# Kernel optimization log

Hardware: AMD Instinct MI355X
Metric: run time of the kernel (lower is better)

## Reference

```python
import jax, jax.numpy as jnp
import numpy as np

# --- static config (mirrors init_kwargs) ---
B, N, CBEV = 4, 4, 64
D, FH, FW = 41, 16, 44          # depth bins, feature H/W after downsample
OGH, OGW, DS = 256, 704, 16     # original image dims, downsample
NX, NY, NZ = 240, 240, 1        # BEV grid (x, y, z)
DX = np.array([0.4, 0.4, 20.0], np.float32)            # voxel size
BX = np.array([-47.8, -47.8, 0.0], np.float32)          # voxel grid origin (bound+dx/2)


def _frustum():
    # [D, FH, FW, 3] with (u_pixel, v_pixel, depth); UD discretization 4..44 step 1
    ds = (4.0 + np.arange(D, dtype=np.float32)).reshape(D, 1, 1) * np.ones((1, FH, FW), np.float32)
    xs = np.linspace(0.0, OGW - 1, FW, dtype=np.float32).reshape(1, 1, FW) * np.ones((D, FH, 1), np.float32)
    ys = np.linspace(0.0, OGH - 1, FH, dtype=np.float32).reshape(1, FH, 1) * np.ones((D, 1, FW), np.float32)
    return jnp.asarray(np.stack([xs, ys, ds], axis=-1))


def setup_inputs() -> dict:
    key = jax.random.key(0)
    x = jax.random.normal(key, (B, N, D, FH, FW, CBEV), dtype=jnp.float32)
    # realistic camera rig: 4 cameras at yaw 0/90/180/270 deg, pinhole intrinsics
    intr = np.zeros((N, 3, 3), np.float32)
    rot = np.zeros((N, 3, 3), np.float32)
    tr = np.zeros((N, 3), np.float32)
    cam2ego = np.array([[0, 0, 1], [-1, 0, 0], [0, -1, 0]], np.float32)  # cam z-fwd -> ego x-fwd
    for n in range(N):
        intr[n] = np.array([[500.0, 0.0, OGW / 2.0], [0.0, 500.0, OGH / 2.0], [0.0, 0.0, 1.0]], np.float32)
        yaw = 2.0 * np.pi * n / N
        c, s = np.cos(yaw), np.sin(yaw)
        Rz = np.array([[c, -s, 0], [s, c, 0], [0, 0, 1]], np.float32)
        rot[n] = Rz @ cam2ego
        tr[n] = np.array([1.5 * c, 1.5 * s, 1.6], np.float32)
    rots = jnp.asarray(np.broadcast_to(rot, (B, N, 3, 3)).copy())
    trans = jnp.asarray(np.broadcast_to(tr, (B, N, 3)).copy())
    intrins = jnp.asarray(np.broadcast_to(intr, (B, N, 3, 3)).copy())
    post_rots = jnp.asarray(np.broadcast_to(np.eye(3, dtype=np.float32), (B, N, 3, 3)).copy())
    post_trans = jnp.zeros((B, N, 3), jnp.float32)
    return {"x": x, "rots": rots, "trans": trans, "intrins": intrins,
            "post_rots": post_rots, "post_trans": post_trans}


def reference(x, rots, trans, intrins, post_rots, post_trans):
    # --- get_geometry: frustum pixel/depth points -> ego-frame xyz ---
    frustum = _frustum()                                            # [D,FH,FW,3]
    pts = frustum[None, None] - post_trans[:, :, None, None, None, :]
    pts = jnp.einsum('bnij,bndhwj->bndhwi', jnp.linalg.inv(post_rots), pts)
    pts = jnp.concatenate([pts[..., :2] * pts[..., 2:3], pts[..., 2:3]], axis=-1)
    combine = rots @ jnp.linalg.inv(intrins)
    pts = jnp.einsum('bnij,bndhwj->bndhwi', combine, pts) + trans[:, :, None, None, None, :]
    # --- voxel_pooling: quantize, mask OOB, segment-sum into dense BEV grid ---
    dx = jnp.asarray(DX)
    bx = jnp.asarray(BX)
    vox = ((pts - (bx - dx / 2.0)) / dx).astype(jnp.int32)          # trunc, same as torch .long()
    vx, vy, vz = vox[..., 0], vox[..., 1], vox[..., 2]              # [B,N,D,FH,FW]
    kept = (vx >= 0) & (vx < NX) & (vy >= 0) & (vy < NY) & (vz >= 0) & (vz < NZ)
    bidx = jnp.arange(B, dtype=jnp.int32)[:, None, None, None, None]
    nvox = B * NZ * NY * NX
    lin = bidx * (NZ * NY * NX) + vz * (NY * NX) + vy * NX + vx
    lin = jnp.where(kept, lin, nvox).reshape(-1)                    # invalid -> dummy bin
    feats = x.reshape(-1, CBEV)                                     # [Nprime, C]
    sums = jax.ops.segment_sum(feats, lin, num_segments=nvox + 1)[:nvox]
    final = sums.reshape(B, NZ, NY, NX, CBEV).transpose(0, 1, 4, 2, 3)  # [B,Z,C,Y,X]
    # torch: cat(final.unbind(dim=2), 1) on [B,C,Z,Y,X] -> [B, Z*C, Y, X] z-major
    return final.reshape(B, NZ * CBEV, NY, NX)
```

## Files before the change

kernel.cpp:

```cpp
#include <hip/hip_runtime.h>

#define BB   4
#define NNC  4
#define DDEP 41
#define FHH  16
#define FWW  44
#define CC   64
#define NXX  240
#define NYY  240
#define NVOX (BB*NYY*NXX)
#define NTRI (BB*NNC*DDEP*FWW)
#define SLOTS 8

#define W_CNT  0
#define W_TAB  (NVOX)

typedef float f4 __attribute__((ext_vector_type(4)));

__device__ __forceinline__ void inv3x3_upper_f32(const float K[9], float o[9]) {
    float a00 = __fdiv_rn(1.0f, K[0]);
    float a11 = __fdiv_rn(1.0f, K[4]);
    float a22 = __fdiv_rn(1.0f, K[8]);
    float b01 = __fmul_rn(-a11, __fmul_rn(a00, K[1]));
    float x0 = __fadd_rn(__fmul_rn(a00, K[2]), __fmul_rn(b01, K[5]));
    float x1 = __fmul_rn(a11, K[5]);
    float b02 = __fmul_rn(-a22, x0);
    float b12 = __fmul_rn(-a22, x1);
    o[0]=a00; o[1]=b01; o[2]=b02;
    o[3]=0.0f; o[4]=a11; o[5]=b12;
    o[6]=0.0f; o[7]=0.0f; o[8]=a22;
}

__global__ void __launch_bounds__(256) geom(
        const float* __restrict__ rots,
        const float* __restrict__ trans,
        const float* __restrict__ intrins,
        const float* __restrict__ post_rots,
        const float* __restrict__ post_trans,
        unsigned int* __restrict__ cntp,
        unsigned int* __restrict__ table) {
    int wid  = threadIdx.x >> 6;
    int lane = threadIdx.x & 63;
    int sub  = lane >> 4;
    int h    = lane & 15;
    int tri  = (blockIdx.x*4 + wid)*4 + sub;

    int w    = tri % FWW;
    int rest = tri / FWW;
    int d    = rest % DDEP;
    int bn   = rest / DDEP;

    float K[9], PR[9], R[9];
    #pragma unroll
    for (int i = 0; i < 9; ++i) {
        K[i]  = intrins[bn*9 + i];
        PR[i] = post_rots[bn*9 + i];
        R[i]  = rots[bn*9 + i];
    }
    float Ki[9], PRi[9];
    inv3x3_upper_f32(K, Ki);
    inv3x3_upper_f32(PR, PRi);
    float C[9];
    #pragma unroll
    for (int i = 0; i < 3; ++i)
        #pragma unroll
        for (int j = 0; j < 3; ++j) {
            float s = __fmul_rn(R[i*3+0], Ki[0*3+j]);
            s = __fadd_rn(s, __fmul_rn(R[i*3+1], Ki[1*3+j]));
            s = __fadd_rn(s, __fmul_rn(R[i*3+2], Ki[2*3+j]));
            C[i*3+j] = s;
        }
    float ptx = post_trans[bn*3+0], pty = post_trans[bn*3+1], ptz = post_trans[bn*3+2];
    float trx = trans[bn*3+0], try_ = trans[bn*3+1], trz = trans[bn*3+2];

    float u  = (float)((double)w * (703.0/43.0));
    float v  = (float)((double)h * 17.0);
    float dd = (float)(4 + d);

    float p0x = __fsub_rn(u,  ptx);
    float p0y = __fsub_rn(v,  pty);
    float p0z = __fsub_rn(dd, ptz);
    float p1x = __fadd_rn(__fadd_rn(__fmul_rn(PRi[0],p0x), __fmul_rn(PRi[1],p0y)), __fmul_rn(PRi[2],p0z));
    float p1y = __fadd_rn(__fadd_rn(__fmul_rn(PRi[3],p0x), __fmul_rn(PRi[4],p0y)), __fmul_rn(PRi[5],p0z));
    float p1z = __fadd_rn(__fadd_rn(__fmul_rn(PRi[6],p0x), __fmul_rn(PRi[7],p0y)), __fmul_rn(PRi[8],p0z));
    float p2x = __fmul_rn(p1x, p1z);
    float p2y = __fmul_rn(p1y, p1z);
    float p2z = p1z;
    float ex = __fadd_rn(__fadd_rn(__fmul_rn(C[0],p2x), __fmul_rn(C[1],p2y)), __fmul_rn(C[2],p2z));
    float ey = __fadd_rn(__fadd_rn(__fmul_rn(C[3],p2x), __fmul_rn(C[4],p2y)), __fmul_rn(C[5],p2z));
    float ez = __fadd_rn(__fadd_rn(__fmul_rn(C[6],p2x), __fmul_rn(C[7],p2y)), __fmul_rn(C[8],p2z));
    float gx = __fadd_rn(ex, trx);
    float gy = __fadd_rn(ey, try_);
    float gz = __fadd_rn(ez, trz);

    float qx = __fdiv_rn(__fsub_rn(gx, -48.0f), 0.4f);
    float qy = __fdiv_rn(__fsub_rn(gy, -48.0f), 0.4f);
    float qz = __fdiv_rn(__fsub_rn(gz, -10.0f), 20.0f);
    int vx = (int)qx;
    int vy = (int)qy;
    int vz = (int)qz;

    bool kept = (vx >= 0) & (vx < NXX) & (vy >= 0) & (vy < NYY) & (vz == 0);
    unsigned long long bal = __ballot(kept);
    unsigned int mask = (unsigned int)((bal >> (sub*16)) & 0xFFFFull);

    if (h == 0 && mask != 0) {
        int b  = bn / NNC;
        int vb = b*(NYY*NXX) + vy*NXX + vx;
        unsigned int sh  = 8u*(vb & 3);
        unsigned int old = atomicAdd(&cntp[vb >> 2], 1u << sh);
        unsigned int sl  = (old >> sh) & 0xFFu;
        if (sl < SLOTS) table[vb*SLOTS + sl] = ((unsigned int)tri << 16) | mask;
    }
}

__global__ void __launch_bounds__(256) assemble(
        const float* __restrict__ x,
        const unsigned int* __restrict__ cntp,
        const unsigned int* __restrict__ table,
        float* __restrict__ out) {
    __shared__ float lds[16*68];
    int tid = threadIdx.x;
    int v0  = blockIdx.x*16;

    const uint4 cq = *(const uint4*)(cntp + (v0 >> 2));

    int b  = v0 / (NYY*NXX);
    int yx = v0 % (NYY*NXX);
    int c  = tid >> 2, q = tid & 3;
    float* outp = out + (size_t)b*(CC*NYY*NXX) + (size_t)c*(NYY*NXX) + yx + q*4;

    if ((cq.x | cq.y | cq.z | cq.w) == 0u) {
        f4 z = (f4)(0.0f);
        __builtin_nontemporal_store(z, (f4*)outp);
        return;
    }

    int wid  = tid >> 6;
    int lane = tid & 63;
    int hq   = lane >> 4;
    int c4   = lane & 15;

    unsigned int cw = (wid & 2) ? ((wid & 1) ? cq.w : cq.z)
                                : ((wid & 1) ? cq.y : cq.x);

    int nk[4]; unsigned int entk[4];
    #pragma unroll
    for (int k = 0; k < 4; ++k) {
        int n = (int)((cw >> (8*k)) & 0xFFu); if (n > SLOTS) n = SLOTS;
        nk[k] = n;
        int cell = v0 + wid*4 + k;
        entk[k] = (lane < n) ? table[cell*SLOTS + lane] : 0u;
    }

    #pragma unroll
    for (int k = 0; k < 4; ++k) {
        f4 acc = (f4)(0.0f);
        int n = nk[k];
        for (int i = 0; i < n; ++i) {
            unsigned int e = (unsigned int)__shfl((int)entk[k], i);
            int tri  = (int)(e >> 16);
            unsigned int m = e & 0xFFFFu;
            int w    = tri % FWW;
            int rest = tri / FWW;
            int d    = rest % DDEP;
            int bn   = rest / DDEP;
            const float* xb = x + (size_t)((bn*DDEP + d)*FHH*FWW + w)*CC + c4*4;
            #pragma unroll
            for (int r = 0; r < 4; ++r) {
                int h = r*4 + hq;
                if ((m >> h) & 1u) {
                    f4 t = *(const f4*)(xb + (size_t)h*(FWW*CC));
                    acc += t;
                }
            }
        }
        acc.x += __shfl_xor(acc.x, 16); acc.y += __shfl_xor(acc.y, 16);
        acc.z += __shfl_xor(acc.z, 16); acc.w += __shfl_xor(acc.w, 16);
        acc.x += __shfl_xor(acc.x, 32); acc.y += __shfl_xor(acc.y, 32);
        acc.z += __shfl_xor(acc.z, 32); acc.w += __shfl_xor(acc.w, 32);
        if (lane < 16)
            *(f4*)&lds[(wid*4 + k)*68 + lane*4] = acc;
    }
    __syncthreads();

    f4 f;
    f.x = lds[(q*4 + 0)*68 + c];
    f.y = lds[(q*4 + 1)*68 + c];
    f.z = lds[(q*4 + 2)*68 + c];
    f.w = lds[(q*4 + 3)*68 + c];
    __builtin_nontemporal_store(f, (f4*)outp);
}

extern "C" void kernel_launch(void* const* d_in, const int* in_sizes, int n_in,
                              void* d_out, int out_size, void* d_ws, size_t ws_size,
                              hipStream_t stream) {
    const float* x          = (const float*)d_in[0];
    const float* rots       = (const float*)d_in[1];
    const float* trans      = (const float*)d_in[2];
    const float* intrins    = (const float*)d_in[3];
    const float* post_rots  = (const float*)d_in[4];
    const float* post_trans = (const float*)d_in[5];
    float* out = (float*)d_out;

    char* ws = (char*)d_ws;
    unsigned int* cntp  = (unsigned int*)(ws + W_CNT);
    unsigned int* table = (unsigned int*)(ws + W_TAB);

    hipMemsetAsync(cntp, 0, NVOX, stream);
    geom<<<NTRI/16, 256, 0, stream>>>(rots, trans, intrins, post_rots, post_trans,
                                      cntp, table);
    assemble<<<NVOX/16, 256, 0, stream>>>(x, cntp, table, out);
}
```

Baseline: 232.0 us.

## Assemble one BEV row per block with dirty-group work distribution across waves

The assemble kernel now has each block handle a full BEV row of 240 cells instead of 16 cells. It scans the row's count words with one ballot and writes zeros for empty 16-cell groups with coalesced stores. Non-empty groups are dealt round-robin to the four waves, and each wave transposes through its own LDS slice. This cuts the launch to 960 blocks, removes per-block overhead and __syncthreads, and balances the sparse work. The risk is fewer blocks, less parallelism and load imbalance when dirty groups cluster in some rows.

```diff
diff --git a/kernel.cpp b/kernel.cpp
--- a/kernel.cpp
+++ b/kernel.cpp
@@ -119,77 +119,98 @@
         const unsigned int* __restrict__ cntp,
         const unsigned int* __restrict__ table,
         float* __restrict__ out) {
-    __shared__ float lds[16*68];
-    int tid = threadIdx.x;
-    int v0  = blockIdx.x*16;
-
-    const uint4 cq = *(const uint4*)(cntp + (v0 >> 2));
-
-    int b  = v0 / (NYY*NXX);
-    int yx = v0 % (NYY*NXX);
-    int c  = tid >> 2, q = tid & 3;
-    float* outp = out + (size_t)b*(CC*NYY*NXX) + (size_t)c*(NYY*NXX) + yx + q*4;
-
-    if ((cq.x | cq.y | cq.z | cq.w) == 0u) {
+    __shared__ float lds[4][16*68];
+    int tid  = threadIdx.x;
+    int lane = tid & 63;
+    int wid  = tid >> 6;
+    int row  = blockIdx.x;
+    int cellbase = row * NXX;
+    int b   = row / NYY;
+    int rowoff = (row - b*NYY) * NXX;
+    float* outb = out + (size_t)b*(CC*NYY*NXX);
+
+    unsigned int cword = (lane < 60) ? cntp[(cellbase >> 2) + lane] : 0u;
+    unsigned long long nz = __ballot(cword != 0u);
+    unsigned int dirty = 0u;
+    #pragma unroll
+    for (int g = 0; g < 15; ++g)
+        dirty |= ((((unsigned int)(nz >> (4*g))) & 0xFu) ? 1u : 0u) << g;
+
+    {
         f4 z = (f4)(0.0f);
-        __builtin_nontemporal_store(z, (f4*)outp);
-        return;
-    }
-
-    int wid  = tid >> 6;
-    int lane = tid & 63;
-    int hq   = lane >> 4;
-    int c4   = lane & 15;
-
-    unsigned int cw = (wid & 2) ? ((wid & 1) ? cq.w : cq.z)
-                                : ((wid & 1) ? cq.y : cq.x);
-
-    int nk[4]; unsigned int entk[4];
-    #pragma unroll
-    for (int k = 0; k < 4; ++k) {
-        int n = (int)((cw >> (8*k)) & 0xFFu); if (n > SLOTS) n = SLOTS;
-        nk[k] = n;
-        int cell = v0 + wid*4 + k;
-        entk[k] = (lane < n) ? table[cell*SLOTS + lane] : 0u;
-    }
-
-    #pragma unroll
-    for (int k = 0; k < 4; ++k) {
-        f4 acc = (f4)(0.0f);
-        int n = nk[k];
-        for (int i = 0; i < n; ++i) {
-            unsigned int e = (unsigned int)__shfl((int)entk[k], i);
-            int tri  = (int)(e >> 16);
-            unsigned int m = e & 0xFFFFu;
-            int w    = tri % FWW;
-            int rest = tri / FWW;
-            int d    = rest % DDEP;
-            int bn   = rest / DDEP;
-            const float* xb = x + (size_t)((bn*DDEP + d)*FHH*FWW + w)*CC + c4*4;
-            #pragma unroll
-            for (int r = 0; r < 4; ++r) {
-                int h = r*4 + hq;
-                if ((m >> h) & 1u) {
-                    f4 t = *(const f4*)(xb + (size_t)h*(FWW*CC));
-                    acc += t;
+        #pragma unroll
+        for (int i = 0; i < 15; ++i) {
+            int s = i*256 + tid;
+            int c = s / 60;
+            int r = s - c*60;
+            if (!((dirty >> (r >> 2)) & 1u))
+                __builtin_nontemporal_store(z,
+                    (f4*)(outb + (size_t)c*(NYY*NXX) + rowoff + r*4));
+        }
+    }
+
+    float* ldsw = &lds[wid][0];
+    int hq = lane >> 4;
+    int c4 = lane & 15;
+    unsigned int dmask = dirty;
+    int gi = 0;
+    while (dmask) {
+        int g = __ffs(dmask) - 1;
+        dmask &= dmask - 1;
+        if ((gi++ & 3) != wid) continue;
+
+        int v0 = cellbase + g*16;
+        const uint4 cq = *(const uint4*)(cntp + (v0 >> 2));
+        unsigned long long cnt_lo = (unsigned long long)cq.x | ((unsigned long long)cq.y << 32);
+        unsigned long long cnt_hi = (unsigned long long)cq.z | ((unsigned long long)cq.w << 32);
+        unsigned int ent0 = table[(size_t)v0*SLOTS + lane];
+        unsigned int ent1 = table[(size_t)v0*SLOTS + 64 + lane];
+
+        #pragma unroll 2
+        for (int k = 0; k < 16; ++k) {
+            unsigned long long cw = (k < 8) ? cnt_lo : cnt_hi;
+            int n = (int)((cw >> (8*(k & 7))) & 0xFFull); if (n > SLOTS) n = SLOTS;
+            f4 acc = (f4)(0.0f);
+            for (int i = 0; i < n; ++i) {
+                int slot = k*SLOTS + i;
+                unsigned int e = (unsigned int)__shfl(
+                    (int)((slot < 64) ? ent0 : ent1), slot & 63);
+                int tri  = (int)(e >> 16);
+                unsigned int m = e & 0xFFFFu;
+                int w    = tri % FWW;
+                int rest = tri / FWW;
+                int d    = rest % DDEP;
+                int bn   = rest / DDEP;
+                const float* xb = x + (size_t)((bn*DDEP + d)*FHH*FWW + w)*CC + c4*4;
+                #pragma unroll
+                for (int r = 0; r < 4; ++r) {
+                    int h = r*4 + hq;
+                    if ((m >> h) & 1u) {
+                        f4 t = *(const f4*)(xb + (size_t)h*(FWW*CC));
+                        acc += t;
+                    }
                 }
             }
-        }
-        acc.x += __shfl_xor(acc.x, 16); acc.y += __shfl_xor(acc.y, 16);
-        acc.z += __shfl_xor(acc.z, 16); acc.w += __shfl_xor(acc.w, 16);
-        acc.x += __shfl_xor(acc.x, 32); acc.y += __shfl_xor(acc.y, 32);
-        acc.z += __shfl_xor(acc.z, 32); acc.w += __shfl_xor(acc.w, 32);
-        if (lane < 16)
-            *(f4*)&lds[(wid*4 + k)*68 + lane*4] = acc;
-    }
-    __syncthreads();
-
-    f4 f;
-    f.x = lds[(q*4 + 0)*68 + c];
-    f.y = lds[(q*4 + 1)*68 + c];
-    f.z = lds[(q*4 + 2)*68 + c];
-    f.w = lds[(q*4 + 3)*68 + c];
-    __builtin_nontemporal_store(f, (f4*)outp);
+            acc.x += __shfl_xor(acc.x, 16); acc.y += __shfl_xor(acc.y, 16);
+            acc.z += __shfl_xor(acc.z, 16); acc.w += __shfl_xor(acc.w, 16);
+            acc.x += __shfl_xor(acc.x, 32); acc.y += __shfl_xor(acc.y, 32);
+            acc.z += __shfl_xor(acc.z, 32); acc.w += __shfl_xor(acc.w, 32);
+            if (lane < 16)
+                *(f4*)&ldsw[k*68 + lane*4] = acc;
+        }
+        #pragma unroll
+        for (int p = 0; p < 4; ++p) {
+            int c = p*16 + (lane >> 2);
+            int q = lane & 3;
+            f4 f;
+            f.x = ldsw[(q*4 + 0)*68 + c];
+            f.y = ldsw[(q*4 + 1)*68 + c];
+            f.z = ldsw[(q*4 + 2)*68 + c];
+            f.w = ldsw[(q*4 + 3)*68 + c];
+            __builtin_nontemporal_store(f,
+                (f4*)(outb + (size_t)c*(NYY*NXX) + rowoff + g*16 + q*4));
+        }
+    }
 }
 
 extern "C" void kernel_launch(void* const* d_in, const int* in_sizes, int n_in,
@@ -210,5 +231,5 @@
     hipMemsetAsync(cntp, 0, NVOX, stream);
     geom<<<NTRI/16, 256, 0, stream>>>(rots, trans, intrins, post_rots, post_trans,
                                       cntp, table);
-    assemble<<<NVOX/16, 256, 0, stream>>>(x, cntp, table, out);
-}
+    assemble<<<BB*NYY, 256, 0, stream>>>(x, cntp, table, out);
+}
```

New measurement: 293.7 us. +26.6%, slower.

## Assemble 64 cells per block with ballot-compacted nonempty cells across waves

Applied to the files above, without the earlier changes.

Each assemble block now covers 64 BEV cells instead of 16. A ballot over the per-cell counts finds the nonempty cells, and these are dealt round-robin to the four waves, so waves no longer walk empty cells. Output rows become 256-byte contiguous stores per channel rather than 64-byte ones. The cost is a larger padded LDS tile that every nonempty block must zero, and possible load imbalance when a block has only a few occupied cells.

```diff
diff --git a/kernel.cpp b/kernel.cpp
--- a/kernel.cpp
+++ b/kernel.cpp
@@ -119,46 +119,48 @@
         const unsigned int* __restrict__ cntp,
         const unsigned int* __restrict__ table,
         float* __restrict__ out) {
-    __shared__ float lds[16*68];
-    int tid = threadIdx.x;
-    int v0  = blockIdx.x*16;
-
-    const uint4 cq = *(const uint4*)(cntp + (v0 >> 2));
-
-    int b  = v0 / (NYY*NXX);
-    int yx = v0 % (NYY*NXX);
-    int c  = tid >> 2, q = tid & 3;
-    float* outp = out + (size_t)b*(CC*NYY*NXX) + (size_t)c*(NYY*NXX) + yx + q*4;
-
-    if ((cq.x | cq.y | cq.z | cq.w) == 0u) {
+    __shared__ float lds[64*65];
+    int tid  = threadIdx.x;
+    int lane = tid & 63;
+    int wid  = tid >> 6;
+    int v0   = blockIdx.x * 64;
+    int b    = v0 / (NYY*NXX);
+    int yx0  = v0 - b*(NYY*NXX);
+    float* outb = out + (size_t)b*(CC*NYY*NXX) + yx0;
+
+    unsigned int cword = cntp[(v0 >> 2) + (lane >> 2)];
+    unsigned int cbyte = (cword >> (8*(lane & 3))) & 0xFFu;
+    unsigned long long dmask = __ballot(cbyte != 0u);
+
+    int sub = lane >> 4, xi = lane & 15;
+
+    if (dmask == 0ull) {
         f4 z = (f4)(0.0f);
-        __builtin_nontemporal_store(z, (f4*)outp);
+        #pragma unroll
+        for (int it = 0; it < 4; ++it) {
+            int c = wid*16 + it*4 + sub;
+            __builtin_nontemporal_store(z, (f4*)(outb + (size_t)c*(NYY*NXX) + xi*4));
+        }
         return;
     }
 
-    int wid  = tid >> 6;
-    int lane = tid & 63;
-    int hq   = lane >> 4;
-    int c4   = lane & 15;
-
-    unsigned int cw = (wid & 2) ? ((wid & 1) ? cq.w : cq.z)
-                                : ((wid & 1) ? cq.y : cq.x);
-
-    int nk[4]; unsigned int entk[4];
-    #pragma unroll
-    for (int k = 0; k < 4; ++k) {
-        int n = (int)((cw >> (8*k)) & 0xFFu); if (n > SLOTS) n = SLOTS;
-        nk[k] = n;
-        int cell = v0 + wid*4 + k;
-        entk[k] = (lane < n) ? table[cell*SLOTS + lane] : 0u;
-    }
-
-    #pragma unroll
-    for (int k = 0; k < 4; ++k) {
+    for (int i = tid; i < 64*65; i += 256) lds[i] = 0.0f;
+
+    int hq = lane >> 4, c4 = lane & 15;
+    unsigned long long m2 = dmask;
+    int gi = 0;
+    while (m2) {
+        int cell = __ffsll((unsigned long long)m2) - 1;
+        m2 &= m2 - 1;
+        if ((gi++ & 3) != wid) continue;
+
+        int n = __shfl((int)cbyte, cell);
+        if (n > SLOTS) n = SLOTS;
+        unsigned int ent = (lane < n) ? table[(size_t)(v0 + cell)*SLOTS + lane] : 0u;
+
         f4 acc = (f4)(0.0f);
-        int n = nk[k];
         for (int i = 0; i < n; ++i) {
-            unsigned int e = (unsigned int)__shfl((int)entk[k], i);
+            unsigned int e = (unsigned int)__shfl((int)ent, i);
             int tri  = (int)(e >> 16);
             unsigned int m = e & 0xFFFFu;
             int w    = tri % FWW;
@@ -179,17 +181,25 @@
         acc.z += __shfl_xor(acc.z, 16); acc.w += __shfl_xor(acc.w, 16);
         acc.x += __shfl_xor(acc.x, 32); acc.y += __shfl_xor(acc.y, 32);
         acc.z += __shfl_xor(acc.z, 32); acc.w += __shfl_xor(acc.w, 32);
-        if (lane < 16)
-            *(f4*)&lds[(wid*4 + k)*68 + lane*4] = acc;
+        if (lane < 16) {
+            lds[cell*65 + c4*4 + 0] = acc.x;
+            lds[cell*65 + c4*4 + 1] = acc.y;
+            lds[cell*65 + c4*4 + 2] = acc.z;
+            lds[cell*65 + c4*4 + 3] = acc.w;
+        }
     }
     __syncthreads();
 
-    f4 f;
-    f.x = lds[(q*4 + 0)*68 + c];
-    f.y = lds[(q*4 + 1)*68 + c];
-    f.z = lds[(q*4 + 2)*68 + c];
-    f.w = lds[(q*4 + 3)*68 + c];
-    __builtin_nontemporal_store(f, (f4*)outp);
+    #pragma unroll
+    for (int it = 0; it < 4; ++it) {
+        int c = wid*16 + it*4 + sub;
+        f4 f;
+        f.x = lds[(xi*4 + 0)*65 + c];
+        f.y = lds[(xi*4 + 1)*65 + c];
+        f.z = lds[(xi*4 + 2)*65 + c];
+        f.w = lds[(xi*4 + 3)*65 + c];
+        __builtin_nontemporal_store(f, (f4*)(outb + (size_t)c*(NYY*NXX) + xi*4));
+    }
 }
 
 extern "C" void kernel_launch(void* const* d_in, const int* in_sizes, int n_in,
@@ -210,5 +220,5 @@
     hipMemsetAsync(cntp, 0, NVOX, stream);
     geom<<<NTRI/16, 256, 0, stream>>>(rots, trans, intrins, post_rots, post_trans,
                                       cntp, table);
-    assemble<<<NVOX/16, 256, 0, stream>>>(x, cntp, table, out);
-}
+    assemble<<<NVOX/64, 256, 0, stream>>>(x, cntp, table, out);
+}
```

Measured after the change: 227.8 us. About the same (-1.8%).

## Compact occupied voxels into a list and split gather from dense writeout

Applied to the files above, without the earlier changes.

The geometry kernel now gives each occupied voxel a compact id, recorded in a list and in a reverse map. A new colsum kernel runs one wavefront per occupied voxel, sums its features into a compact scratch buffer, and skips empty cells. A separate writeout kernel fills the dense output in channel-major rows with a swizzled block order, reading scratch only for occupied cells. The aim is to avoid launching gather work for empty voxel tiles and to keep output writes contiguous, at the cost of an extra launch, more atomics and a scratch round trip.

```diff
diff --git a/kernel.cpp b/kernel.cpp
--- a/kernel.cpp
+++ b/kernel.cpp
@@ -12,8 +12,12 @@
 #define NTRI (BB*NNC*DDEP*FWW)
 #define SLOTS 8
 
-#define W_CNT  0
-#define W_TAB  (NVOX)
+#define W_CNT 0
+#define W_CTR (NVOX)
+#define W_VBL (W_CTR + 16)
+#define W_CID (W_VBL + NTRI*4)
+#define W_TAB (W_CID + NVOX*2)
+#define W_SCR (W_TAB + NVOX*SLOTS*4)
 
 typedef float f4 __attribute__((ext_vector_type(4)));
 
@@ -38,7 +42,10 @@
         const float* __restrict__ post_rots,
         const float* __restrict__ post_trans,
         unsigned int* __restrict__ cntp,
-        unsigned int* __restrict__ table) {
+        unsigned int* __restrict__ table,
+        unsigned int* __restrict__ ctr,
+        unsigned int* __restrict__ vblist,
+        unsigned short* __restrict__ cidmap) {
     int wid  = threadIdx.x >> 6;
     int lane = threadIdx.x & 63;
     int sub  = lane >> 4;
@@ -110,86 +117,91 @@
         unsigned int sh  = 8u*(vb & 3);
         unsigned int old = atomicAdd(&cntp[vb >> 2], 1u << sh);
         unsigned int sl  = (old >> sh) & 0xFFu;
+        if (sl == 0u) {
+            unsigned int id = atomicAdd(ctr, 1u);
+            cidmap[vb] = (unsigned short)id;
+            vblist[id] = (unsigned int)vb;
+        }
         if (sl < SLOTS) table[vb*SLOTS + sl] = ((unsigned int)tri << 16) | mask;
     }
 }
 
-__global__ void __launch_bounds__(256) assemble(
+__global__ void __launch_bounds__(256) colsum(
         const float* __restrict__ x,
         const unsigned int* __restrict__ cntp,
         const unsigned int* __restrict__ table,
+        const unsigned int* __restrict__ ctr,
+        const unsigned int* __restrict__ vblist,
+        float* __restrict__ scratch) {
+    int lane = threadIdx.x & 63;
+    int wid  = threadIdx.x >> 6;
+    unsigned int cid = blockIdx.x*4 + wid;
+    if (cid >= ctr[0]) return;
+
+    int vb = (int)vblist[cid];
+    int n  = (int)((cntp[vb >> 2] >> (8*(vb & 3))) & 0xFFu);
+    if (n > SLOTS) n = SLOTS;
+    unsigned int ent = (lane < n) ? table[(size_t)vb*SLOTS + lane] : 0u;
+
+    int hq = lane >> 4, c4 = lane & 15;
+    f4 acc = (f4)(0.0f);
+    for (int i = 0; i < n; ++i) {
+        unsigned int e = (unsigned int)__shfl((int)ent, i);
+        int tri  = (int)(e >> 16);
+        unsigned int m = e & 0xFFFFu;
+        int w    = tri % FWW;
+        int rest = tri / FWW;
+        int d    = rest % DDEP;
+        int bn   = rest / DDEP;
+        const float* xb = x + (size_t)((bn*DDEP + d)*FHH*FWW + w)*CC + c4*4;
+        #pragma unroll
+        for (int r = 0; r < 4; ++r) {
+            int h = r*4 + hq;
+            if ((m >> h) & 1u) {
+                f4 t = *(const f4*)(xb + (size_t)h*(FWW*CC));
+                acc += t;
+            }
+        }
+    }
+    acc.x += __shfl_xor(acc.x, 16); acc.y += __shfl_xor(acc.y, 16);
+    acc.z += __shfl_xor(acc.z, 16); acc.w += __shfl_xor(acc.w, 16);
+    acc.x += __shfl_xor(acc.x, 32); acc.y += __shfl_xor(acc.y, 32);
+    acc.z += __shfl_xor(acc.z, 32); acc.w += __shfl_xor(acc.w, 32);
+    if (lane < 16)
+        *(f4*)&scratch[(size_t)cid*CC + c4*4] = acc;
+}
+
+__global__ void __launch_bounds__(256) writeout(
+        const unsigned int* __restrict__ cntp,
+        const unsigned short* __restrict__ cidmap,
+        const float* __restrict__ scratch,
         float* __restrict__ out) {
-    __shared__ float lds[16*68];
-    int tid = threadIdx.x;
-    int v0  = blockIdx.x*16;
-
-    const uint4 cq = *(const uint4*)(cntp + (v0 >> 2));
-
-    int b  = v0 / (NYY*NXX);
-    int yx = v0 % (NYY*NXX);
-    int c  = tid >> 2, q = tid & 3;
-    float* outp = out + (size_t)b*(CC*NYY*NXX) + (size_t)c*(NYY*NXX) + yx + q*4;
-
-    if ((cq.x | cq.y | cq.z | cq.w) == 0u) {
-        f4 z = (f4)(0.0f);
-        __builtin_nontemporal_store(z, (f4*)outp);
-        return;
-    }
-
-    int wid  = tid >> 6;
-    int lane = tid & 63;
-    int hq   = lane >> 4;
-    int c4   = lane & 15;
-
-    unsigned int cw = (wid & 2) ? ((wid & 1) ? cq.w : cq.z)
-                                : ((wid & 1) ? cq.y : cq.x);
-
-    int nk[4]; unsigned int entk[4];
-    #pragma unroll
-    for (int k = 0; k < 4; ++k) {
-        int n = (int)((cw >> (8*k)) & 0xFFu); if (n > SLOTS) n = SLOTS;
-        nk[k] = n;
-        int cell = v0 + wid*4 + k;
-        entk[k] = (lane < n) ? table[cell*SLOTS + lane] : 0u;
-    }
-
-    #pragma unroll
-    for (int k = 0; k < 4; ++k) {
-        f4 acc = (f4)(0.0f);
-        int n = nk[k];
-        for (int i = 0; i < n; ++i) {
-            unsigned int e = (unsigned int)__shfl((int)entk[k], i);
-            int tri  = (int)(e >> 16);
-            unsigned int m = e & 0xFFFFu;
-            int w    = tri % FWW;
-            int rest = tri / FWW;
-            int d    = rest % DDEP;
-            int bn   = rest / DDEP;
-            const float* xb = x + (size_t)((bn*DDEP + d)*FHH*FWW + w)*CC + c4*4;
-            #pragma unroll
-            for (int r = 0; r < 4; ++r) {
-                int h = r*4 + hq;
-                if ((m >> h) & 1u) {
-                    f4 t = *(const f4*)(xb + (size_t)h*(FWW*CC));
-                    acc += t;
-                }
+    int nb  = BB*CC*60;
+    int bid = blockIdx.x;
+    int swz = (bid & 7)*(nb >> 3) + (bid >> 3);
+    int y4  = swz % 60;
+    int rc  = swz / 60;
+    int c   = rc & 63;
+    int b   = rc >> 6;
+
+    int t = threadIdx.x;
+    if (t >= 240) return;
+
+    int cellbase = b*(NYY*NXX) + y4*960;
+    unsigned int cw = cntp[(cellbase >> 2) + t];
+
+    f4 v = (f4)(0.0f);
+    if (cw != 0u) {
+        #pragma unroll
+        for (int k = 0; k < 4; ++k) {
+            if ((cw >> (8*k)) & 0xFFu) {
+                unsigned int id = cidmap[cellbase + t*4 + k];
+                v[k] = scratch[(size_t)id*CC + c];
             }
         }
-        acc.x += __shfl_xor(acc.x, 16); acc.y += __shfl_xor(acc.y, 16);
-        acc.z += __shfl_xor(acc.z, 16); acc.w += __shfl_xor(acc.w, 16);
-        acc.x += __shfl_xor(acc.x, 32); acc.y += __shfl_xor(acc.y, 32);
-        acc.z += __shfl_xor(acc.z, 32); acc.w += __shfl_xor(acc.w, 32);
-        if (lane < 16)
-            *(f4*)&lds[(wid*4 + k)*68 + lane*4] = acc;
-    }
-    __syncthreads();
-
-    f4 f;
-    f.x = lds[(q*4 + 0)*68 + c];
-    f.y = lds[(q*4 + 1)*68 + c];
-    f.z = lds[(q*4 + 2)*68 + c];
-    f.w = lds[(q*4 + 3)*68 + c];
-    __builtin_nontemporal_store(f, (f4*)outp);
+    }
+    __builtin_nontemporal_store(v,
+        (f4*)(out + (size_t)rc*(NYY*NXX) + y4*960 + t*4));
 }
 
 extern "C" void kernel_launch(void* const* d_in, const int* in_sizes, int n_in,
@@ -204,11 +216,16 @@
     float* out = (float*)d_out;
 
     char* ws = (char*)d_ws;
-    unsigned int* cntp  = (unsigned int*)(ws + W_CNT);
-    unsigned int* table = (unsigned int*)(ws + W_TAB);
-
-    hipMemsetAsync(cntp, 0, NVOX, stream);
+    unsigned int*   cntp    = (unsigned int*)(ws + W_CNT);
+    unsigned int*   ctr     = (unsigned int*)(ws + W_CTR);
+    unsigned int*   vblist  = (unsigned int*)(ws + W_VBL);
+    unsigned short* cidmap  = (unsigned short*)(ws + W_CID);
+    unsigned int*   table   = (unsigned int*)(ws + W_TAB);
+    float*          scratch = (float*)(ws + W_SCR);
+
+    hipMemsetAsync(cntp, 0, NVOX + 16, stream);
     geom<<<NTRI/16, 256, 0, stream>>>(rots, trans, intrins, post_rots, post_trans,
-                                      cntp, table);
-    assemble<<<NVOX/16, 256, 0, stream>>>(x, cntp, table, out);
-}
+                                      cntp, table, ctr, vblist, cidmap);
+    colsum<<<NTRI/4, 256, 0, stream>>>(x, cntp, table, ctr, vblist, scratch);
+    writeout<<<BB*CC*60, 256, 0, stream>>>(cntp, cidmap, scratch, out);
+}
```

Measured after the change: 297.6 us. 28.3% more time.
